# Performance work log

Measured on AMD Instinct MI355X. Metric: run time of the kernel, lower is better.

Reference implementation:

```python
import jax, jax.numpy as jnp
import numpy as np

D_MODEL = 1024
D_HIDDEN = 4096
D_OUT = 1024
N_EXPERTS = 8
TOP_K = 2
LOAD_BALANCE_WEIGHT = 0.01


def setup_inputs() -> dict:
    key = jax.random.key(0)
    ks = jax.random.split(key, 8)
    s = 0.02
    return {
        "input_tensor": jax.random.normal(ks[0], (4, 2048, D_MODEL), dtype=jnp.float32),
        "router_w": jax.random.normal(ks[1], (N_EXPERTS, D_MODEL), dtype=jnp.float32) * s,
        "router_b": jnp.zeros((N_EXPERTS,), dtype=jnp.float32),
        "w1": jax.random.normal(ks[2], (N_EXPERTS, D_HIDDEN, D_MODEL), dtype=jnp.float32) * s,
        "b1": jnp.zeros((N_EXPERTS, D_HIDDEN), dtype=jnp.float32),
        "w2": jax.random.normal(ks[3], (N_EXPERTS, D_OUT, D_HIDDEN), dtype=jnp.float32) * s,
        "b2": jnp.zeros((N_EXPERTS, D_OUT), dtype=jnp.float32),
    }


def _moe(input_tensor, router_w, router_b, w1, b1, w2, b2):
    B, S, D = input_tensor.shape
    x = input_tensor.reshape(-1, D)  # [T, D]
    T = x.shape[0]

    router_logits = x @ router_w.T + router_b          # [T, E]
    router_probs = jax.nn.softmax(router_logits, -1)   # [T, E]
    topk_w, topk_idx = jax.lax.top_k(router_probs, TOP_K)  # [T, K]
    topk_w = topk_w / jnp.sum(topk_w, axis=-1, keepdims=True)

    # Dense combine weights: zero for unselected experts (same math as
    # gather/scatter loop since unselected contributions get weight 0).
    combine = jnp.zeros((T, N_EXPERTS), dtype=topk_w.dtype)
    combine = combine.at[jnp.arange(T)[:, None], topk_idx].add(topk_w)  # [T, E]

    out = jnp.zeros((T, D_OUT), dtype=x.dtype)
    for e in range(N_EXPERTS):  # fixed, small expert loop
        h = jax.nn.relu(x @ w1[e].T + b1[e])      # [T, H]
        y = h @ w2[e].T + b2[e]                   # [T, O]
        out = out + combine[:, e:e + 1] * y
    output = out.reshape(B, S, D_OUT)

    # Load-balance loss
    one_hot = jax.nn.one_hot(topk_idx, N_EXPERTS, dtype=router_probs.dtype)  # [T, K, E]
    usage_frac = jnp.sum(one_hot, axis=(0, 1)) / (T * TOP_K)                 # [E]
    mean_prob = jnp.mean(router_probs, axis=0)                               # [E]
    lb_loss = LOAD_BALANCE_WEIGHT * N_EXPERTS * jnp.sum(usage_frac * mean_prob)
    return output, lb_loss


def reference(input_tensor, router_w, router_b, w1, b1, w2, b2):
    return _moe(input_tensor, router_w, router_b, w1, b1, w2, b2)
```

## Files before the change

kernel.cpp:

```cpp
#include <hip/hip_runtime.h>

typedef unsigned short u16;
typedef __bf16 bf16x8 __attribute__((ext_vector_type(8)));
typedef float f32x4 __attribute__((ext_vector_type(4)));

#define T_TOKENS 8192
#define DM 1024
#define DH 4096
#define DO 1024
#define NE 8

#define XB_OFF   0ull
#define W1B_OFF  16777216ull
#define W2B_OFF  16777216ull
#define H_OFF    83886080ull
#define PT_OFF   218103808ull
#define PG_OFF   218169344ull
#define TI_OFF   218234880ull
#define TG_OFF   218300416ull
#define ST_OFF   218365952ull


typedef __attribute__((address_space(3))) void lds_void;
typedef __attribute__((address_space(1))) const void gbl_void;

__device__ __forceinline__ void gload_lds16(const void* g, void* l) {
  __builtin_amdgcn_global_load_lds((gbl_void*)g, (lds_void*)l, 16, 0, 0);
}

__device__ __forceinline__ u16 f2bf(float f) {
  union { float f; unsigned u; } a; a.f = f;
  unsigned u = a.u;
  return (u16)((u + 0x7FFFu + ((u >> 16) & 1u)) >> 16);
}

__global__ __launch_bounds__(256) void cast_f32_bf16(const float* __restrict__ src,
                                                     u16* __restrict__ dst, int n4) {
  int i = blockIdx.x * 256 + threadIdx.x;
  if (i >= n4) return;
  float4 v = ((const float4*)src)[i];
  ushort4 o;
  o.x = f2bf(v.x); o.y = f2bf(v.y); o.z = f2bf(v.z); o.w = f2bf(v.w);
  ((ushort4*)dst)[i] = o;
}

__global__ __launch_bounds__(256) void router_kernel(
    const float* __restrict__ x, const float* __restrict__ rw,
    const float* __restrict__ rb,
    int* __restrict__ tidx, float* __restrict__ tgate,
    int* __restrict__ counts, float* __restrict__ psum)
{
  __shared__ float srw[NE * DM];
  __shared__ float s_psum[NE];
  __shared__ int s_cnt[NE];

  for (int i = threadIdx.x; i < NE * DM; i += 256) srw[i] = rw[i];
  if (threadIdx.x < NE) { s_psum[threadIdx.x] = 0.f; s_cnt[threadIdx.x] = 0; }
  __syncthreads();

  const int wave = threadIdx.x >> 6;
  const int lane = threadIdx.x & 63;
  const int t = blockIdx.x * 4 + wave;

  float xv[16];
#pragma unroll
  for (int i = 0; i < 16; i++) xv[i] = x[(size_t)t * DM + i * 64 + lane];

  float logits[8];
#pragma unroll
  for (int e = 0; e < 8; e++) {
    float p = 0.f;
#pragma unroll
    for (int i = 0; i < 16; i++) p += xv[i] * srw[e * DM + i * 64 + lane];
#pragma unroll
    for (int o = 32; o > 0; o >>= 1) p += __shfl_xor(p, o, 64);
    logits[e] = p;
  }

  if (lane == 0) {
    float pe[8];
    float mx = -1e30f;
    for (int e = 0; e < 8; e++) { logits[e] += rb[e]; mx = fmaxf(mx, logits[e]); }
    float s = 0.f;
    for (int e = 0; e < 8; e++) { pe[e] = expf(logits[e] - mx); s += pe[e]; }
    float inv = 1.f / s;
    for (int e = 0; e < 8; e++) { pe[e] *= inv; atomicAdd(&s_psum[e], pe[e]); }
    int i0 = 0;
    for (int e = 1; e < 8; e++) if (pe[e] > pe[i0]) i0 = e;
    int i1 = (i0 == 0) ? 1 : 0;
    for (int e = 0; e < 8; e++) if (e != i0 && pe[e] > pe[i1]) i1 = e;
    float g = pe[i0] + pe[i1];
    tidx[t * 2] = i0; tidx[t * 2 + 1] = i1;
    tgate[t * 2] = pe[i0] / g; tgate[t * 2 + 1] = pe[i1] / g;
    atomicAdd(&s_cnt[i0], 1); atomicAdd(&s_cnt[i1], 1);
  }
  __syncthreads();
  if (threadIdx.x < NE) {
    atomicAdd(&counts[threadIdx.x], s_cnt[threadIdx.x]);
    atomicAdd(&psum[threadIdx.x], s_psum[threadIdx.x]);
  }
}

__global__ void offsets_kernel(const int* __restrict__ counts, int* __restrict__ offs) {
  if (threadIdx.x == 0) {
    int a = 0;
    for (int e = 0; e < NE; e++) { offs[e] = a; a += counts[e]; }
  }
}

__global__ __launch_bounds__(256) void scatter_kernel(
    const int* __restrict__ tidx, const float* __restrict__ tgate,
    const int* __restrict__ offs, int* __restrict__ cursor,
    int* __restrict__ ptok, float* __restrict__ pgate)
{
  int t = blockIdx.x * 256 + threadIdx.x;
#pragma unroll
  for (int k = 0; k < 2; k++) {
    int e = tidx[t * 2 + k];
    int pos = offs[e] + atomicAdd(&cursor[e], 1);
    ptok[pos] = t;
    pgate[pos] = tgate[t * 2 + k];
  }
}


#define GEMM_CORE_DECLS                                                        \
  __shared__ __align__(16) u16 sm[16384];        \
  const int tid = threadIdx.x;                                                 \
  const int lane = tid & 63;                                                   \
  const int wave = tid >> 6;                                                   \
  const int wm = wave & 1, wn = wave >> 1;                                     \
  const int q = lane >> 4, ml = lane & 15;                                     \
  const int schunk = (tid & 3) ^ ((tid >> 3) & 3);     \
  const int srow = tid >> 2;                                \
  const int fsw = (q ^ ((ml >> 1) & 3)) * 8;      \
  int offA[4], offB[4];                                                        \
  _Pragma("unroll") for (int t4 = 0; t4 < 4; t4++) {                           \
    offA[t4] = (wm * 64 + t4 * 16 + ml) * 32 + fsw;                            \
    offB[t4] = 4096 + (wn * 64 + t4 * 16 + ml) * 32 + fsw;                     \
  }                                                                            \
  const f32x4 z = {0.f, 0.f, 0.f, 0.f};                                        \
  f32x4 acc[4][4];                                                             \
  _Pragma("unroll") for (int i = 0; i < 4; i++)                                \
    _Pragma("unroll") for (int j = 0; j < 4; j++) acc[i][j] = z;

#define GEMM_STAGE(buf, k0)                                                    \
  {                                                                            \
    u16* dst = sm + (buf) * 8192 + tid * 8;                                    \
    gload_lds16(aptr0 + (k0), dst);                                            \
    gload_lds16(aptr1 + (k0), dst + 2048);                                     \
    gload_lds16(bptr0 + (k0), dst + 4096);                                     \
    gload_lds16(bptr1 + (k0), dst + 6144);                                     \
  }

#define GEMM_KLOOP(KD)                                                         \
  GEMM_STAGE(0, 0)                                                             \
  int cur = 0;                                                                 \
  for (int k0 = 0; k0 < (KD); k0 += 32) {                                      \
    __syncthreads();                                                           \
    if (k0 + 32 < (KD)) { GEMM_STAGE(cur ^ 1, k0 + 32) }                       \
    const u16* Ab = sm + cur * 8192;                                           \
    bf16x8 af[4], bv[4];                                                       \
    _Pragma("unroll") for (int mt = 0; mt < 4; mt++)                           \
      af[mt] = *(const bf16x8*)&Ab[offA[mt]];                                  \
    _Pragma("unroll") for (int nt = 0; nt < 4; nt++)                           \
      bv[nt] = *(const bf16x8*)&Ab[offB[nt]];                                  \
    _Pragma("unroll") for (int mt = 0; mt < 4; mt++)                           \
      _Pragma("unroll") for (int nt = 0; nt < 4; nt++)                         \
        acc[mt][nt] =                                                          \
            __builtin_amdgcn_mfma_f32_16x16x32_bf16(af[mt], bv[nt],            \
                                                    acc[mt][nt], 0, 0, 0);     \
    cur ^= 1;                                                                  \
  }

__global__ __launch_bounds__(256) void gemm1_kernel(
    const u16* __restrict__ xb, const u16* __restrict__ w1b,
    const float* __restrict__ b1, const int* __restrict__ ptok,
    const int* __restrict__ offs, const int* __restrict__ counts,
    u16* __restrict__ h)
{
  const int e = blockIdx.z;
  const int cnt = counts[e];
  const int row0 = blockIdx.y * 128;
  if (row0 >= cnt) return;
  const int off = offs[e];
  const int col0 = blockIdx.x * 128;

  GEMM_CORE_DECLS

  int ra0 = row0 + srow, ra1 = row0 + 64 + srow;
  int tk0 = ptok[off + (ra0 < cnt ? ra0 : 0)];
  int tk1 = ptok[off + (ra1 < cnt ? ra1 : 0)];
  const u16* aptr0 = xb + (size_t)tk0 * DM + schunk * 8;
  const u16* aptr1 = xb + (size_t)tk1 * DM + schunk * 8;
  const u16* bptr0 = w1b + ((size_t)e * DH + col0 + srow) * DM + schunk * 8;
  const u16* bptr1 = w1b + ((size_t)e * DH + col0 + 64 + srow) * DM + schunk * 8;

  GEMM_KLOOP(DM)

#pragma unroll
  for (int mt = 0; mt < 4; mt++) {
#pragma unroll
    for (int reg = 0; reg < 4; reg++) {
      int prow = row0 + wm * 64 + mt * 16 + q * 4 + reg;
      if (prow < cnt) {
#pragma unroll
        for (int nt = 0; nt < 4; nt++) {
          int gcol = col0 + wn * 64 + nt * 16 + ml;
          float v = acc[mt][nt][reg] + b1[e * DH + gcol];
          v = fmaxf(v, 0.f);
          h[(size_t)(off + prow) * DH + gcol] = f2bf(v);
        }
      }
    }
  }
}

__global__ __launch_bounds__(256) void gemm2_kernel(
    const u16* __restrict__ h, const u16* __restrict__ w2b,
    const float* __restrict__ b2, const int* __restrict__ ptok,
    const float* __restrict__ pgate,
    const int* __restrict__ offs, const int* __restrict__ counts,
    float* __restrict__ out)
{
  const int e = blockIdx.z;
  const int cnt = counts[e];
  const int row0 = blockIdx.y * 128;
  if (row0 >= cnt) return;
  const int off = offs[e];
  const int col0 = blockIdx.x * 128;

  GEMM_CORE_DECLS

  int ra0 = row0 + srow, ra1 = row0 + 64 + srow;
  int ar0 = off + (ra0 < cnt ? ra0 : 0);
  int ar1 = off + (ra1 < cnt ? ra1 : 0);
  const u16* aptr0 = h + (size_t)ar0 * DH + schunk * 8;
  const u16* aptr1 = h + (size_t)ar1 * DH + schunk * 8;
  const u16* bptr0 = w2b + ((size_t)e * DO + col0 + srow) * DH + schunk * 8;
  const u16* bptr1 = w2b + ((size_t)e * DO + col0 + 64 + srow) * DH + schunk * 8;

  GEMM_KLOOP(DH)

#pragma unroll
  for (int mt = 0; mt < 4; mt++) {
#pragma unroll
    for (int reg = 0; reg < 4; reg++) {
      int prow = row0 + wm * 64 + mt * 16 + q * 4 + reg;
      if (prow < cnt) {
        int t = ptok[off + prow];
        float g = pgate[off + prow];
#pragma unroll
        for (int nt = 0; nt < 4; nt++) {
          int gcol = col0 + wn * 64 + nt * 16 + ml;
          float v = acc[mt][nt][reg] + b2[e * DO + gcol];
          atomicAdd(&out[(size_t)t * DO + gcol], g * v);
        }
      }
    }
  }
}

__global__ void loss_kernel(const int* __restrict__ counts, const float* __restrict__ psum,
                            float* __restrict__ out, size_t idx, int T) {
  if (threadIdx.x == 0 && blockIdx.x == 0) {
    float s = 0.f;
    for (int e = 0; e < NE; e++)
      s += ((float)counts[e] / (float)(T * 2)) * (psum[e] / (float)T);
    out[idx] = 0.01f * 8.0f * s;
  }
}

extern "C" void kernel_launch(void* const* d_in, const int* in_sizes, int n_in,
                              void* d_out, int out_size, void* d_ws, size_t ws_size,
                              hipStream_t stream) {
  const float* x  = (const float*)d_in[0];
  const float* rw = (const float*)d_in[1];
  const float* rb = (const float*)d_in[2];
  const float* w1 = (const float*)d_in[3];
  const float* b1 = (const float*)d_in[4];
  const float* w2 = (const float*)d_in[5];
  const float* b2 = (const float*)d_in[6];
  float* out = (float*)d_out;
  char* ws = (char*)d_ws;

  u16* xb    = (u16*)(ws + XB_OFF);
  u16* w1b   = (u16*)(ws + W1B_OFF);
  u16* w2b   = (u16*)(ws + W2B_OFF);
  u16* h     = (u16*)(ws + H_OFF);
  int* ptok  = (int*)(ws + PT_OFF);
  float* pgate = (float*)(ws + PG_OFF);
  int* tidx  = (int*)(ws + TI_OFF);
  float* tgate = (float*)(ws + TG_OFF);
  int* counts = (int*)(ws + ST_OFF);
  int* cursor = (int*)(ws + ST_OFF + 32);
  int* offs   = (int*)(ws + ST_OFF + 64);
  float* psum = (float*)(ws + ST_OFF + 96);

  hipMemsetAsync(d_out, 0, (size_t)out_size * sizeof(float), stream);
  hipMemsetAsync(ws + ST_OFF, 0, 256, stream);

  cast_f32_bf16<<<(T_TOKENS * DM / 4 + 255) / 256, 256, 0, stream>>>(x, xb, T_TOKENS * DM / 4);
  cast_f32_bf16<<<(NE * DH * DM / 4 + 255) / 256, 256, 0, stream>>>(w1, w1b, NE * DH * DM / 4);

  router_kernel<<<T_TOKENS / 4, 256, 0, stream>>>(x, rw, rb, tidx, tgate, counts, psum);
  offsets_kernel<<<1, 64, 0, stream>>>(counts, offs);
  scatter_kernel<<<T_TOKENS / 256, 256, 0, stream>>>(tidx, tgate, offs, cursor, ptok, pgate);

  gemm1_kernel<<<dim3(DH / 128, T_TOKENS / 128, NE), 256, 0, stream>>>(
      xb, w1b, b1, ptok, offs, counts, h);

  cast_f32_bf16<<<(NE * DO * DH / 4 + 255) / 256, 256, 0, stream>>>(w2, w2b, NE * DO * DH / 4);

  gemm2_kernel<<<dim3(DO / 128, T_TOKENS / 128, NE), 256, 0, stream>>>(
      h, w2b, b2, ptok, pgate, offs, counts, out);

  loss_kernel<<<1, 1, 0, stream>>>(counts, psum, out, (size_t)out_size - 1, T_TOKENS);
}
```

Measured before the change: 909.9 us.

## Use 256x256 ping-pong MoE GEMM tiles and atomic-free output combine

Both expert GEMMs move from 128x128 tiles with 256 threads to 256x256 tiles with 512 threads. Each step loads a 64-wide K slice into a double-buffered 128KB LDS area. MFMA quarters are interleaved with async global-to-LDS staging, explicit barriers, vmcnt waits and setprio, with the aim of raising data reuse and overlapping loads with math. The second GEMM can write gated per-slot rows to a workspace buffer, and a new combine kernel sums each token's two rows, replacing float atomics and the output memset. The cost is large LDS use that limits occupancy, extra workspace traffic, and a dependence on the workspace being large enough.

```diff
diff --git a/kernel.cpp b/kernel.cpp
--- a/kernel.cpp
+++ b/kernel.cpp
@@ -19,7 +19,8 @@
 #define TI_OFF   218234880ull
 #define TG_OFF   218300416ull
 #define ST_OFF   218365952ull
-
+#define YW_OFF   218370048ull
+#define YW_SZ    67108864ull
 
 typedef __attribute__((address_space(3))) void lds_void;
 typedef __attribute__((address_space(1))) const void gbl_void;
@@ -109,71 +110,122 @@
 }
 
 __global__ __launch_bounds__(256) void scatter_kernel(
-    const int* __restrict__ tidx, const float* __restrict__ tgate,
+    const int* tidx, const float* __restrict__ tgate,
     const int* __restrict__ offs, int* __restrict__ cursor,
-    int* __restrict__ ptok, float* __restrict__ pgate)
+    int* __restrict__ ptok, float* __restrict__ pgate, int* ppos)
 {
   int t = blockIdx.x * 256 + threadIdx.x;
-#pragma unroll
-  for (int k = 0; k < 2; k++) {
-    int e = tidx[t * 2 + k];
-    int pos = offs[e] + atomicAdd(&cursor[e], 1);
-    ptok[pos] = t;
-    pgate[pos] = tgate[t * 2 + k];
-  }
-}
-
-
-#define GEMM_CORE_DECLS                                                        \
-  __shared__ __align__(16) u16 sm[16384];        \
+  int e0 = tidx[t * 2], e1 = tidx[t * 2 + 1];
+  float g0 = tgate[t * 2], g1 = tgate[t * 2 + 1];
+  int p0 = offs[e0] + atomicAdd(&cursor[e0], 1);
+  int p1 = offs[e1] + atomicAdd(&cursor[e1], 1);
+  ptok[p0] = t; pgate[p0] = g0;
+  ptok[p1] = t; pgate[p1] = g1;
+  ppos[t * 2] = p0; ppos[t * 2 + 1] = p1;
+}
+
+
+#define FENCE asm volatile("" ::: "memory")
+#define BAR  do { FENCE; __builtin_amdgcn_s_barrier(); FENCE; } while (0)
+#define VMW4 asm volatile("s_waitcnt vmcnt(4)" ::: "memory")
+#define VMW0 asm volatile("s_waitcnt vmcnt(0)" ::: "memory")
+
+#define G256_DECLS                                                             \
+  __shared__ __align__(16) u16 sm[65536];                         \
   const int tid = threadIdx.x;                                                 \
   const int lane = tid & 63;                                                   \
   const int wave = tid >> 6;                                                   \
   const int wm = wave & 1, wn = wave >> 1;                                     \
   const int q = lane >> 4, ml = lane & 15;                                     \
-  const int schunk = (tid & 3) ^ ((tid >> 3) & 3);     \
-  const int srow = tid >> 2;                                \
-  const int fsw = (q ^ ((ml >> 1) & 3)) * 8;      \
-  int offA[4], offB[4];                                                        \
-  _Pragma("unroll") for (int t4 = 0; t4 < 4; t4++) {                           \
-    offA[t4] = (wm * 64 + t4 * 16 + ml) * 32 + fsw;                            \
-    offB[t4] = 4096 + (wn * 64 + t4 * 16 + ml) * 32 + fsw;                     \
+  const int swz0 = (q ^ (ml & 7)) * 8;             \
+  const int swz1 = ((4 + q) ^ (ml & 7)) * 8;                   \
+  const int baseA = wm * 8192 + ml * 64;                                       \
+  const int baseB = 16384 + (wn >> 1) * 8192 + (wn & 1) * 4096 + ml * 64;      \
+  const int cs = ((tid & 7) ^ ((tid >> 3) & 7)) * 8;    \
+  const int srow = tid >> 3;          \
+  f32x4 acc[8][4];                                                             \
+  { const f32x4 z_ = {0.f, 0.f, 0.f, 0.f};                                     \
+    _Pragma("unroll") for (int i_ = 0; i_ < 8; i_++)                           \
+      _Pragma("unroll") for (int j_ = 0; j_ < 4; j_++) acc[i_][j_] = z_; }     \
+  bf16x8 areg[4][2], breg[4][2];
+
+#define STAGE_A(buf, half, k0)                                                 \
+  { u16* d_ = sm + (buf) * 32768 + (half) * 8192 + tid * 8;                    \
+    gload_lds16(aP[half][0] + (k0), d_);                                       \
+    gload_lds16(aP[half][1] + (k0), d_ + 4096); }
+
+#define STAGE_B(buf, half, k0, KD)                                             \
+  { u16* d_ = sm + (buf) * 32768 + 16384 + (half) * 8192 + tid * 8;            \
+    gload_lds16(bB + (size_t)((half) * 128) * (KD) + (k0), d_);                \
+    gload_lds16(bB + (size_t)((half) * 128 + 64) * (KD) + (k0), d_ + 4096); }
+
+#define READ_A(buf, mh)                                                        \
+  _Pragma("unroll") for (int m_ = 0; m_ < 4; m_++) {                           \
+    areg[m_][0] = *(const bf16x8*)&sm[(buf) * 32768 + baseA +                  \
+                                      ((mh) * 4 + m_) * 1024 + swz0];          \
+    areg[m_][1] = *(const bf16x8*)&sm[(buf) * 32768 + baseA +                  \
+                                      ((mh) * 4 + m_) * 1024 + swz1];          \
+  }
+
+#define READ_B(buf, nh)                                                        \
+  _Pragma("unroll") for (int n_ = 0; n_ < 2; n_++) {                           \
+    breg[(nh) * 2 + n_][0] = *(const bf16x8*)&sm[(buf) * 32768 + baseB +       \
+                                      ((nh) * 2 + n_) * 1024 + swz0];          \
+    breg[(nh) * 2 + n_][1] = *(const bf16x8*)&sm[(buf) * 32768 + baseB +       \
+                                      ((nh) * 2 + n_) * 1024 + swz1];          \
+  }
+
+#define MFMA_Q(mh, nh)                                                         \
+  __builtin_amdgcn_s_setprio(1);                                               \
+  _Pragma("unroll") for (int m_ = 0; m_ < 4; m_++)                             \
+    _Pragma("unroll") for (int n_ = 0; n_ < 2; n_++) {                         \
+      acc[(mh)*4+m_][(nh)*2+n_] = __builtin_amdgcn_mfma_f32_16x16x32_bf16(     \
+          areg[m_][0], breg[(nh)*2+n_][0], acc[(mh)*4+m_][(nh)*2+n_], 0,0,0);  \
+      acc[(mh)*4+m_][(nh)*2+n_] = __builtin_amdgcn_mfma_f32_16x16x32_bf16(     \
+          areg[m_][1], breg[(nh)*2+n_][1], acc[(mh)*4+m_][(nh)*2+n_], 0,0,0);  \
+    }                                                                          \
+  __builtin_amdgcn_s_setprio(0);
+
+#define G256_ITER(KD, k1, k2, k3, ST)                                          \
+  READ_A(0, 0) READ_B(0, 0)                                                    \
+  STAGE_A(1, 1, (k1))                                                          \
+  BAR; MFMA_Q(0, 0) BAR;                                                       \
+  READ_B(0, 1)                                                                 \
+  STAGE_B(1, 1, (k1), KD)                                                      \
+  BAR; MFMA_Q(0, 1) BAR;                                                       \
+  READ_A(0, 1)                                                                 \
+  if (ST) STAGE_B(0, 0, (k2), KD)                                              \
+  BAR; MFMA_Q(1, 1) BAR;                                                       \
+  if (ST) STAGE_A(0, 0, (k2))                                                  \
+  BAR; MFMA_Q(1, 0)                                                            \
+  if (ST) { VMW4; } else { VMW0; }                                             \
+  BAR;                                                                         \
+  READ_A(1, 0) READ_B(1, 0)                                                    \
+  if (ST) STAGE_A(0, 1, (k2))                                                  \
+  BAR; MFMA_Q(0, 0) BAR;                                                       \
+  READ_B(1, 1)                                                                 \
+  if (ST) STAGE_B(0, 1, (k2), KD)                                              \
+  BAR; MFMA_Q(0, 1) BAR;                                                       \
+  READ_A(1, 1)                                                                 \
+  if (ST) STAGE_B(1, 0, (k3), KD)                                              \
+  BAR; MFMA_Q(1, 1) BAR;                                                       \
+  if (ST) STAGE_A(1, 0, (k3))                                                  \
+  BAR; MFMA_Q(1, 0)                                                            \
+  if (ST) { VMW4; }                                                            \
+  BAR;
+
+#define G256_KLOOP(KD)                                                         \
+  STAGE_B(0, 0, 0, KD) STAGE_A(0, 0, 0)                                        \
+  STAGE_A(0, 1, 0) STAGE_B(0, 1, 0, KD)                                        \
+  STAGE_B(1, 0, 64, KD) STAGE_A(1, 0, 64)                                      \
+  VMW4; BAR;                                                                   \
+  for (int it_ = 0; it_ < (KD) / 128 - 1; ++it_) {                             \
+    const int kb_ = it_ * 128;                                                 \
+    G256_ITER(KD, kb_ + 64, kb_ + 128, kb_ + 192, 1)                           \
   }                                                                            \
-  const f32x4 z = {0.f, 0.f, 0.f, 0.f};                                        \
-  f32x4 acc[4][4];                                                             \
-  _Pragma("unroll") for (int i = 0; i < 4; i++)                                \
-    _Pragma("unroll") for (int j = 0; j < 4; j++) acc[i][j] = z;
-
-#define GEMM_STAGE(buf, k0)                                                    \
-  {                                                                            \
-    u16* dst = sm + (buf) * 8192 + tid * 8;                                    \
-    gload_lds16(aptr0 + (k0), dst);                                            \
-    gload_lds16(aptr1 + (k0), dst + 2048);                                     \
-    gload_lds16(bptr0 + (k0), dst + 4096);                                     \
-    gload_lds16(bptr1 + (k0), dst + 6144);                                     \
-  }
-
-#define GEMM_KLOOP(KD)                                                         \
-  GEMM_STAGE(0, 0)                                                             \
-  int cur = 0;                                                                 \
-  for (int k0 = 0; k0 < (KD); k0 += 32) {                                      \
-    __syncthreads();                                                           \
-    if (k0 + 32 < (KD)) { GEMM_STAGE(cur ^ 1, k0 + 32) }                       \
-    const u16* Ab = sm + cur * 8192;                                           \
-    bf16x8 af[4], bv[4];                                                       \
-    _Pragma("unroll") for (int mt = 0; mt < 4; mt++)                           \
-      af[mt] = *(const bf16x8*)&Ab[offA[mt]];                                  \
-    _Pragma("unroll") for (int nt = 0; nt < 4; nt++)                           \
-      bv[nt] = *(const bf16x8*)&Ab[offB[nt]];                                  \
-    _Pragma("unroll") for (int mt = 0; mt < 4; mt++)                           \
-      _Pragma("unroll") for (int nt = 0; nt < 4; nt++)                         \
-        acc[mt][nt] =                                                          \
-            __builtin_amdgcn_mfma_f32_16x16x32_bf16(af[mt], bv[nt],            \
-                                                    acc[mt][nt], 0, 0, 0);     \
-    cur ^= 1;                                                                  \
-  }
-
-__global__ __launch_bounds__(256) void gemm1_kernel(
+  G256_ITER(KD, (KD) - 64, 0, 0, 0)
+
+__global__ __launch_bounds__(512, 2) void gemm1_kernel(
     const u16* __restrict__ xb, const u16* __restrict__ w1b,
     const float* __restrict__ b1, const int* __restrict__ ptok,
     const int* __restrict__ offs, const int* __restrict__ counts,
@@ -181,84 +233,110 @@
 {
   const int e = blockIdx.z;
   const int cnt = counts[e];
-  const int row0 = blockIdx.y * 128;
+  const int row0 = blockIdx.y * 256;
   if (row0 >= cnt) return;
   const int off = offs[e];
-  const int col0 = blockIdx.x * 128;
-
-  GEMM_CORE_DECLS
-
-  int ra0 = row0 + srow, ra1 = row0 + 64 + srow;
-  int tk0 = ptok[off + (ra0 < cnt ? ra0 : 0)];
-  int tk1 = ptok[off + (ra1 < cnt ? ra1 : 0)];
-  const u16* aptr0 = xb + (size_t)tk0 * DM + schunk * 8;
-  const u16* aptr1 = xb + (size_t)tk1 * DM + schunk * 8;
-  const u16* bptr0 = w1b + ((size_t)e * DH + col0 + srow) * DM + schunk * 8;
-  const u16* bptr1 = w1b + ((size_t)e * DH + col0 + 64 + srow) * DM + schunk * 8;
-
-  GEMM_KLOOP(DM)
-
-#pragma unroll
-  for (int mt = 0; mt < 4; mt++) {
-#pragma unroll
-    for (int reg = 0; reg < 4; reg++) {
-      int prow = row0 + wm * 64 + mt * 16 + q * 4 + reg;
+  const int col0 = blockIdx.x * 256;
+
+  G256_DECLS
+
+  const u16* aP[2][2];
+#pragma unroll
+  for (int a_ = 0; a_ < 2; a_++)
+#pragma unroll
+    for (int j_ = 0; j_ < 2; j_++) {
+      int p = row0 + a_ * 128 + srow + j_ * 64;
+      int tk = ptok[off + (p < cnt ? p : 0)];
+      aP[a_][j_] = xb + (size_t)tk * DM + cs;
+    }
+  const u16* bB = w1b + ((size_t)e * DH + col0 + srow) * DM + cs;
+
+  G256_KLOOP(DM)
+
+#pragma unroll
+  for (int M = 0; M < 8; M++) {
+#pragma unroll
+    for (int r_ = 0; r_ < 4; r_++) {
+      int prow = row0 + wm * 128 + M * 16 + q * 4 + r_;
       if (prow < cnt) {
 #pragma unroll
-        for (int nt = 0; nt < 4; nt++) {
-          int gcol = col0 + wn * 64 + nt * 16 + ml;
-          float v = acc[mt][nt][reg] + b1[e * DH + gcol];
-          v = fmaxf(v, 0.f);
-          h[(size_t)(off + prow) * DH + gcol] = f2bf(v);
+        for (int N = 0; N < 4; N++) {
+          int gcol = col0 + wn * 64 + N * 16 + ml;
+          float v = acc[M][N][r_] + b1[e * DH + gcol];
+          h[(size_t)(off + prow) * DH + gcol] = f2bf(fmaxf(v, 0.f));
         }
       }
     }
   }
 }
 
-__global__ __launch_bounds__(256) void gemm2_kernel(
+__global__ __launch_bounds__(512, 2) void gemm2_kernel(
     const u16* __restrict__ h, const u16* __restrict__ w2b,
     const float* __restrict__ b2, const int* __restrict__ ptok,
     const float* __restrict__ pgate,
     const int* __restrict__ offs, const int* __restrict__ counts,
-    float* __restrict__ out)
+    float* __restrict__ yw, float* __restrict__ out, int use_yw)
 {
   const int e = blockIdx.z;
   const int cnt = counts[e];
-  const int row0 = blockIdx.y * 128;
+  const int row0 = blockIdx.y * 256;
   if (row0 >= cnt) return;
   const int off = offs[e];
-  const int col0 = blockIdx.x * 128;
-
-  GEMM_CORE_DECLS
-
-  int ra0 = row0 + srow, ra1 = row0 + 64 + srow;
-  int ar0 = off + (ra0 < cnt ? ra0 : 0);
-  int ar1 = off + (ra1 < cnt ? ra1 : 0);
-  const u16* aptr0 = h + (size_t)ar0 * DH + schunk * 8;
-  const u16* aptr1 = h + (size_t)ar1 * DH + schunk * 8;
-  const u16* bptr0 = w2b + ((size_t)e * DO + col0 + srow) * DH + schunk * 8;
-  const u16* bptr1 = w2b + ((size_t)e * DO + col0 + 64 + srow) * DH + schunk * 8;
-
-  GEMM_KLOOP(DH)
-
-#pragma unroll
-  for (int mt = 0; mt < 4; mt++) {
-#pragma unroll
-    for (int reg = 0; reg < 4; reg++) {
-      int prow = row0 + wm * 64 + mt * 16 + q * 4 + reg;
+  const int col0 = blockIdx.x * 256;
+
+  G256_DECLS
+
+  const u16* aP[2][2];
+#pragma unroll
+  for (int a_ = 0; a_ < 2; a_++)
+#pragma unroll
+    for (int j_ = 0; j_ < 2; j_++) {
+      int p = row0 + a_ * 128 + srow + j_ * 64;
+      aP[a_][j_] = h + (size_t)(off + (p < cnt ? p : 0)) * DH + cs;
+    }
+  const u16* bB = w2b + ((size_t)e * DO + col0 + srow) * DH + cs;
+
+  G256_KLOOP(DH)
+
+#pragma unroll
+  for (int M = 0; M < 8; M++) {
+#pragma unroll
+    for (int r_ = 0; r_ < 4; r_++) {
+      int prow = row0 + wm * 128 + M * 16 + q * 4 + r_;
       if (prow < cnt) {
-        int t = ptok[off + prow];
-        float g = pgate[off + prow];
-#pragma unroll
-        for (int nt = 0; nt < 4; nt++) {
-          int gcol = col0 + wn * 64 + nt * 16 + ml;
-          float v = acc[mt][nt][reg] + b2[e * DO + gcol];
-          atomicAdd(&out[(size_t)t * DO + gcol], g * v);
+        int pr = off + prow;
+        float g = pgate[pr];
+        if (use_yw) {
+#pragma unroll
+          for (int N = 0; N < 4; N++) {
+            int gcol = col0 + wn * 64 + N * 16 + ml;
+            yw[(size_t)pr * DO + gcol] = g * (acc[M][N][r_] + b2[e * DO + gcol]);
+          }
+        } else {
+          int t = ptok[pr];
+#pragma unroll
+          for (int N = 0; N < 4; N++) {
+            int gcol = col0 + wn * 64 + N * 16 + ml;
+            atomicAdd(&out[(size_t)t * DO + gcol], g * (acc[M][N][r_] + b2[e * DO + gcol]));
+          }
         }
       }
     }
   }
+}
+
+__global__ __launch_bounds__(256) void combine_kernel(
+    const float* __restrict__ yw, const int* __restrict__ ppos,
+    float* __restrict__ out)
+{
+  int t = blockIdx.x;
+  int j = threadIdx.x;
+  int p0 = ppos[t * 2], p1 = ppos[t * 2 + 1];
+  float4 a = ((const float4*)(yw + (size_t)p0 * DO))[j];
+  float4 b = ((const float4*)(yw + (size_t)p1 * DO))[j];
+  float4 o;
+  o.x = a.x + b.x; o.y = a.y + b.y; o.z = a.z + b.z; o.w = a.w + b.w;
+  ((float4*)(out + (size_t)t * DO))[j] = o;
 }
 
 __global__ void loss_kernel(const int* __restrict__ counts, const float* __restrict__ psum,
@@ -296,8 +374,13 @@
   int* cursor = (int*)(ws + ST_OFF + 32);
   int* offs   = (int*)(ws + ST_OFF + 64);
   float* psum = (float*)(ws + ST_OFF + 96);
-
-  hipMemsetAsync(d_out, 0, (size_t)out_size * sizeof(float), stream);
+  int* ppos   = tidx;
+  float* yw   = (float*)(ws + YW_OFF);
+
+  const bool use_yw = ws_size >= YW_OFF + YW_SZ;
+
+  if (!use_yw)
+    hipMemsetAsync(d_out, 0, (size_t)out_size * sizeof(float), stream);
   hipMemsetAsync(ws + ST_OFF, 0, 256, stream);
 
   cast_f32_bf16<<<(T_TOKENS * DM / 4 + 255) / 256, 256, 0, stream>>>(x, xb, T_TOKENS * DM / 4);
@@ -305,15 +388,17 @@
 
   router_kernel<<<T_TOKENS / 4, 256, 0, stream>>>(x, rw, rb, tidx, tgate, counts, psum);
   offsets_kernel<<<1, 64, 0, stream>>>(counts, offs);
-  scatter_kernel<<<T_TOKENS / 256, 256, 0, stream>>>(tidx, tgate, offs, cursor, ptok, pgate);
-
-  gemm1_kernel<<<dim3(DH / 128, T_TOKENS / 128, NE), 256, 0, stream>>>(
-      xb, w1b, b1, ptok, offs, counts, h);
+  scatter_kernel<<<T_TOKENS / 256, 256, 0, stream>>>(tidx, tgate, offs, cursor, ptok, pgate, ppos);
+
+  gemm1_kernel<<<dim3(DH / 256, 32, NE), 512, 0, stream>>>(xb, w1b, b1, ptok, offs, counts, h);
 
   cast_f32_bf16<<<(NE * DO * DH / 4 + 255) / 256, 256, 0, stream>>>(w2, w2b, NE * DO * DH / 4);
 
-  gemm2_kernel<<<dim3(DO / 128, T_TOKENS / 128, NE), 256, 0, stream>>>(
-      h, w2b, b2, ptok, pgate, offs, counts, out);
+  gemm2_kernel<<<dim3(DO / 256, 32, NE), 512, 0, stream>>>(
+      h, w2b, b2, ptok, pgate, offs, counts, yw, out, use_yw ? 1 : 0);
+
+  if (use_yw)
+    combine_kernel<<<T_TOKENS, 256, 0, stream>>>(yw, ppos, out);
 
   loss_kernel<<<1, 1, 0, stream>>>(counts, psum, out, (size_t)out_size - 1, T_TOKENS);
 }
```

New measurement: 837.0 us. 8.0% less time.
